# Kernel optimization log

Hardware: AMD Instinct MI355X
Metric: run time of the kernel (lower is better)

Reference implementation:

```python
import jax, jax.numpy as jnp
import numpy as np

N_NODES = 20000
N_EDGES = 320000
N_GRAPHS = 64
SEQ = 20
SCALAR = 16
EMB = 32
HID = 128
HEADS = 4
IN_DIM = SCALAR + 5 * EMB  # 176
NEG_SLOPE = 0.2


def masked_mean_embed(table, idx):
    # table: [V, EMB], idx: [N, L] with 0 = padding
    emb = table[idx]                                  # [N, L, EMB]
    mask = (idx != 0).astype(emb.dtype)[..., None]    # [N, L, 1]
    return (emb * mask).sum(axis=1) / (mask.sum(axis=1) + 1e-9)


def gat_conv(x, src, dst, W, att_src, att_dst, bias, heads, out_ch):
    # PyG GATConv (add_self_loops already applied to src/dst), concat heads.
    N = x.shape[0]
    xw = (x @ W).reshape(N, heads, out_ch)            # [N, H, C]
    a_src = (xw * att_src).sum(-1)                    # [N, H]
    a_dst = (xw * att_dst).sum(-1)                    # [N, H]
    e = jax.nn.leaky_relu(a_src[src] + a_dst[dst], NEG_SLOPE)  # [E, H]
    e_max = jax.ops.segment_max(e, dst, num_segments=N)
    e_max = jnp.where(jnp.isfinite(e_max), e_max, 0.0)
    ex = jnp.exp(e - e_max[dst])                      # [E, H]
    denom = jax.ops.segment_sum(ex, dst, num_segments=N)
    alpha = ex / (denom[dst] + 1e-16)                 # [E, H]
    msg = xw[src] * alpha[:, :, None]                 # [E, H, C]
    out = jax.ops.segment_sum(msg, dst, num_segments=N)
    return out.reshape(N, heads * out_ch) + bias


def setup_inputs() -> dict:
    key = jax.random.key(0)
    ks = jax.random.split(key, 24)
    s = 0.05
    inp = {
        "x_scalar": jax.random.normal(ks[0], (N_NODES, SCALAR), jnp.float32),
        "x_opcode": jax.random.randint(ks[1], (N_NODES, SEQ), 0, 256),
        "x_source": jax.random.randint(ks[2], (N_NODES, SEQ), 0, 512),
        "x_sink": jax.random.randint(ks[3], (N_NODES, SEQ), 0, 512),
        "x_string_manip": jax.random.randint(ks[4], (N_NODES, SEQ), 0, 128),
        "x_payload": jax.random.randint(ks[5], (N_NODES, SEQ), 0, 1024),
        "edge_index": jax.random.randint(ks[6], (2, N_EDGES), 0, N_NODES),
        "batch": jnp.sort(jax.random.randint(ks[7], (N_NODES,), 0, N_GRAPHS)),
        # embedding tables (row 0 = padding; masked out anyway)
        "emb_opcode": jax.random.normal(ks[8], (256, EMB)) * s,
        "emb_source": jax.random.normal(ks[9], (512, EMB)) * s,
        "emb_sink": jax.random.normal(ks[10], (512, EMB)) * s,
        "emb_string": jax.random.normal(ks[11], (128, EMB)) * s,
        "emb_payload": jax.random.normal(ks[12], (1024, EMB)) * s,
        "ln_gamma": jnp.ones((IN_DIM,), jnp.float32),
        "ln_beta": jnp.zeros((IN_DIM,), jnp.float32),
        "W1": jax.random.normal(ks[13], (IN_DIM, HEADS * HID)) * s,
        "att_src1": jax.random.normal(ks[14], (HEADS, HID)) * s,
        "att_dst1": jax.random.normal(ks[15], (HEADS, HID)) * s,
        "b1": jnp.zeros((HEADS * HID,), jnp.float32),
        "W2": jax.random.normal(ks[16], (HEADS * HID, HID)) * s,
        "att_src2": jax.random.normal(ks[17], (1, HID)) * s,
        "att_dst2": jax.random.normal(ks[18], (1, HID)) * s,
        "b2": jnp.zeros((HID,), jnp.float32),
        "cls_w1": jax.random.normal(ks[19], (HID, HID // 2)) * s,
        "cls_b1": jnp.zeros((HID // 2,), jnp.float32),
        "cls_w2": jax.random.normal(ks[20], (HID // 2, 2)) * s,
        "cls_b2": jnp.zeros((2,), jnp.float32),
    }
    return inp


def reference(x_scalar, x_opcode, x_source, x_sink, x_string_manip, x_payload,
              edge_index, batch,
              emb_opcode, emb_source, emb_sink, emb_string, emb_payload,
              ln_gamma, ln_beta,
              W1, att_src1, att_dst1, b1,
              W2, att_src2, att_dst2, b2,
              cls_w1, cls_b1, cls_w2, cls_b2):
    feats = jnp.concatenate([
        x_scalar,
        masked_mean_embed(emb_opcode, x_opcode),
        masked_mean_embed(emb_source, x_source),
        masked_mean_embed(emb_sink, x_sink),
        masked_mean_embed(emb_string, x_string_manip),
        masked_mean_embed(emb_payload, x_payload),
    ], axis=1)  # [N, 176]
    mu = feats.mean(-1, keepdims=True)
    var = ((feats - mu) ** 2).mean(-1, keepdims=True)
    h = (feats - mu) / jnp.sqrt(var + 1e-5) * ln_gamma + ln_beta

    # add self loops (PyG GATConv default)
    loops = jnp.arange(N_NODES, dtype=edge_index.dtype)
    src = jnp.concatenate([edge_index[0], loops])
    dst = jnp.concatenate([edge_index[1], loops])

    x = jax.nn.elu(gat_conv(h, src, dst, W1, att_src1, att_dst1, b1, HEADS, HID))
    x = jax.nn.elu(gat_conv(x, src, dst, W2, att_src2, att_dst2, b2, 1, HID))

    pooled = jax.ops.segment_max(x, batch, num_segments=N_GRAPHS)  # [G, HID]
    hcls = jax.nn.relu(pooled @ cls_w1 + cls_b1)
    return hcls @ cls_w2 + cls_b2  # [G, 2]
```

## Files before the change

### kernel.cpp

```cpp
#include <hip/hip_runtime.h>
#include <hip/hip_bf16.h>
#include <math.h>

#define N_NODES 20000
#define N_EDGES 320000
#define N_GRAPHS 64
#define SEQ 20
#define SCALAR 16
#define EMB 32
#define HID 128
#define IN_DIM 176
#define TOT_EDGES (N_EDGES + N_NODES)
#define CHUNK_SMALL 10000
#define POOL_SLICES 32

typedef _Float16 half8v __attribute__((ext_vector_type(8)));
typedef float f32x4 __attribute__((ext_vector_type(4)));
#define LO_SCALE 2048.0f
#define LO_INV (1.0f / 2048.0f)

#define PB2_ELEMS (16 * 8 * 64 * 8)
#define PB1_ELEMS (4 * 6 * 8 * 64 * 8)

#define COUNT_BLOCKS ((TOT_EDGES + 255) / 256)
#define NB4 ((N_NODES + 3) / 4)
#define L1_PACK1 NB4
#define L1_PACK2 (NB4 + 48)
#define L1_COUNT (NB4 + 80)
#define L1_TOTAL (NB4 + 80 + COUNT_BLOCKS + 1)

__device__ inline float readlane_f(float v, int l) {
  return __uint_as_float(__builtin_amdgcn_readlane(__float_as_uint(v), l));
}
__device__ inline int readlane_i(int v, int l) {
  return __builtin_amdgcn_readlane(v, l);
}
__device__ inline float leaky(float e) { return e >= 0.f ? e : 0.2f * e; }
__device__ inline float elu(float v) { return v > 0.f ? v : expf(v) - 1.f; }

__global__ __launch_bounds__(256) void wasd_kernel(
    const float* __restrict__ W1, const float* __restrict__ att_s1,
    const float* __restrict__ att_d1, float* __restrict__ was4,
    float* __restrict__ wad4) {
  int lane = threadIdx.x & 63;
  int k = blockIdx.x * 4 + (threadIdx.x >> 6);
  if (k >= IN_DIM) return;
  const float* wrow = W1 + (size_t)k * 512;
  float s[4], d[4];
#pragma unroll
  for (int hh = 0; hh < 4; ++hh) {
    float w0 = wrow[hh * 128 + lane], w1 = wrow[hh * 128 + 64 + lane];
    float a0 = att_s1[hh * 128 + lane], a1 = att_s1[hh * 128 + 64 + lane];
    float c0 = att_d1[hh * 128 + lane], c1 = att_d1[hh * 128 + 64 + lane];
    s[hh] = w0 * a0 + w1 * a1;
    d[hh] = w0 * c0 + w1 * c1;
  }
  for (int off = 1; off < 64; off <<= 1) {
#pragma unroll
    for (int hh = 0; hh < 4; ++hh) {
      s[hh] += __shfl_xor(s[hh], off);
      d[hh] += __shfl_xor(d[hh], off);
    }
  }
  if (lane == 0) {
    *(float4*)&was4[k * 4] = make_float4(s[0], s[1], s[2], s[3]);
    *(float4*)&wad4[k * 4] = make_float4(d[0], d[1], d[2], d[3]);
  }
}

__global__ __launch_bounds__(256) void feats_setup_kernel(
    const float* __restrict__ xs,
    const int* __restrict__ i0, const int* __restrict__ i1,
    const int* __restrict__ i2, const int* __restrict__ i3,
    const int* __restrict__ i4,
    const float* __restrict__ t0, const float* __restrict__ t1,
    const float* __restrict__ t2, const float* __restrict__ t3,
    const float* __restrict__ t4,
    const float* __restrict__ gamma, const float* __restrict__ beta,
    const float* __restrict__ was4, const float* __restrict__ wad4,
    const float* __restrict__ W1, const float* __restrict__ W2,
    const int* __restrict__ edge_index, const int* __restrict__ batch,
    float* __restrict__ hout, float* __restrict__ a_s,
    float* __restrict__ a_d,
    _Float16* __restrict__ PB1h, _Float16* __restrict__ PB1l,
    _Float16* __restrict__ PB2h, _Float16* __restrict__ PB2l,
    int* __restrict__ cnt, int* __restrict__ gstarts) {
  int b = blockIdx.x;
  if (b >= NB4) {
    if (b < L1_PACK2) {
      int t = (b - L1_PACK1) * 256 + threadIdx.x;
      int lane = t & 63, wi = t >> 6;
      int r = lane & 15, g = lane >> 4;
      int ntile = wi & 7, rem = wi >> 3;
      int ks = rem % 6, hh = rem / 6;
      int col = hh * 128 + ntile * 16 + r;
      size_t o = ((size_t)wi * 64 + lane) * 8;
#pragma unroll
      for (int j = 0; j < 8; ++j) {
        int k = ks * 32 + g * 8 + j;
        float v = (k < IN_DIM) ? W1[(size_t)k * 512 + col] : 0.f;
        _Float16 h = (_Float16)v;
        PB1h[o + j] = h;
        PB1l[o + j] = (_Float16)((v - (float)h) * LO_SCALE);
      }
    } else if (b < L1_COUNT) {
      int t = (b - L1_PACK2) * 256 + threadIdx.x;
      int lane = t & 63, wi = t >> 6;
      int r = lane & 15, g = lane >> 4;
      int ks = wi >> 3, ntile = wi & 7;
      int col = ntile * 16 + r;
      size_t o = ((size_t)wi * 64 + lane) * 8;
#pragma unroll
      for (int j = 0; j < 8; ++j) {
        int k = ks * 32 + g * 8 + j;
        float v = W2[(size_t)k * 128 + col];
        _Float16 h = (_Float16)v;
        PB2h[o + j] = h;
        PB2l[o + j] = (_Float16)((v - (float)h) * LO_SCALE);
      }
    } else if (b < L1_COUNT + COUNT_BLOCKS) {
      int i = (b - L1_COUNT) * 256 + threadIdx.x;
      if (i < N_EDGES) {
        atomicAdd(&cnt[edge_index[N_EDGES + i]], 1);
      } else if (i < TOT_EDGES) {
        atomicAdd(&cnt[i - N_EDGES], 1);
      }
    } else {
      int t = threadIdx.x;
      if (t > N_GRAPHS) return;
      int lo = 0, hi = N_NODES;
      while (lo < hi) {
        int mid = (lo + hi) >> 1;
        if (batch[mid] < t) lo = mid + 1; else hi = mid;
      }
      gstarts[t] = lo;
    }
    return;
  }
  int lane = threadIdx.x & 63;
  int w = threadIdx.x >> 6;
  int n = b * 4 + w;
  if (n >= N_NODES) return;
  __shared__ int sidx[4][100];
  {
    int j = lane;
    int tab = j / 20, l = j - tab * 20;
    const int* ip = tab == 0 ? i0 : tab == 1 ? i1 : tab == 2 ? i2 : i3;
    sidx[w][j] = ip[n * SEQ + l];
    if (lane < 36) {
      int j2 = 64 + lane;
      int tab2 = j2 / 20, l2 = j2 - tab2 * 20;
      const int* ip2 = tab2 == 3 ? i3 : i4;
      sidx[w][j2] = ip2[n * SEQ + l2];
    }
  }
  bool l48 = lane < 48;
  float f0, f1, f2 = 0.f;
  if (lane < SCALAR) {
    f0 = xs[n * SCALAR + lane];
  } else {
    int tt = lane - SCALAR, tab = tt >> 5, d = tt & 31;
    const float* tp = tab == 0 ? t0 : t1;
    float sum = 0.f, cnt2 = 0.f;
#pragma unroll
    for (int l = 0; l < SEQ; ++l) {
      int id = sidx[w][tab * 20 + l];
      if (id != 0) { sum += tp[id * EMB + d]; cnt2 += 1.f; }
    }
    f0 = sum / (cnt2 + 1e-9f);
  }
  {
    int tt = 48 + lane, tab = tt >> 5, d = tt & 31;
    const float* tp = tab == 1 ? t1 : tab == 2 ? t2 : t3;
    float sum = 0.f, cnt2 = 0.f;
#pragma unroll
    for (int l = 0; l < SEQ; ++l) {
      int id = sidx[w][tab * 20 + l];
      if (id != 0) { sum += tp[id * EMB + d]; cnt2 += 1.f; }
    }
    f1 = sum / (cnt2 + 1e-9f);
  }
  if (l48) {
    int tt = 112 + lane, tab = tt >> 5, d = tt & 31;
    const float* tp = tab == 3 ? t3 : t4;
    float sum = 0.f, cnt2 = 0.f;
#pragma unroll
    for (int l = 0; l < SEQ; ++l) {
      int id = sidx[w][tab * 20 + l];
      if (id != 0) { sum += tp[id * EMB + d]; cnt2 += 1.f; }
    }
    f2 = sum / (cnt2 + 1e-9f);
  }
  float s = f0 + f1 + f2;
  for (int off = 1; off < 64; off <<= 1) s += __shfl_xor(s, off);
  float mu = s / (float)IN_DIM;
  float v = (f0 - mu) * (f0 - mu) + (f1 - mu) * (f1 - mu) +
            (l48 ? (f2 - mu) * (f2 - mu) : 0.f);
  for (int off = 1; off < 64; off <<= 1) v += __shfl_xor(v, off);
  float rstd = 1.0f / sqrtf(v / (float)IN_DIM + 1e-5f);
  float hv0 = (f0 - mu) * rstd * gamma[lane] + beta[lane];
  float hv1 = (f1 - mu) * rstd * gamma[64 + lane] + beta[64 + lane];
  float hv2 = l48 ? (f2 - mu) * rstd * gamma[128 + lane] + beta[128 + lane] : 0.f;
  float* hr = hout + (size_t)n * IN_DIM;
  hr[lane] = hv0;
  hr[64 + lane] = hv1;
  if (l48) hr[128 + lane] = hv2;

  const float4* wsv = (const float4*)was4;
  const float4* wdv = (const float4*)wad4;
  float4 wsa = wsv[lane], wsb = wsv[64 + lane];
  float4 wsc = l48 ? wsv[128 + lane] : make_float4(0.f, 0.f, 0.f, 0.f);
  float4 wda = wdv[lane], wdb = wdv[64 + lane];
  float4 wdc = l48 ? wdv[128 + lane] : make_float4(0.f, 0.f, 0.f, 0.f);
  float ps0 = hv0 * wsa.x + hv1 * wsb.x + hv2 * wsc.x;
  float ps1 = hv0 * wsa.y + hv1 * wsb.y + hv2 * wsc.y;
  float ps2 = hv0 * wsa.z + hv1 * wsb.z + hv2 * wsc.z;
  float ps3 = hv0 * wsa.w + hv1 * wsb.w + hv2 * wsc.w;
  float pd0 = hv0 * wda.x + hv1 * wdb.x + hv2 * wdc.x;
  float pd1 = hv0 * wda.y + hv1 * wdb.y + hv2 * wdc.y;
  float pd2 = hv0 * wda.z + hv1 * wdb.z + hv2 * wdc.z;
  float pd3 = hv0 * wda.w + hv1 * wdb.w + hv2 * wdc.w;
  for (int off = 1; off < 64; off <<= 1) {
    ps0 += __shfl_xor(ps0, off); ps1 += __shfl_xor(ps1, off);
    ps2 += __shfl_xor(ps2, off); ps3 += __shfl_xor(ps3, off);
    pd0 += __shfl_xor(pd0, off); pd1 += __shfl_xor(pd1, off);
    pd2 += __shfl_xor(pd2, off); pd3 += __shfl_xor(pd3, off);
  }
  if (lane == 0) {
    *(float4*)&a_s[n * 4] = make_float4(ps0, ps1, ps2, ps3);
    *(float4*)&a_d[n * 4] = make_float4(pd0, pd1, pd2, pd3);
  }
}

__global__ __launch_bounds__(1024) void prefix_kernel(const int* __restrict__ cnt,
                                                      int* __restrict__ indptr,
                                                      int n, int total) {
  __shared__ int ss[1024];
  int t = threadIdx.x;
  int per = (n + 1023) / 1024;
  int beg = t * per, end = min(beg + per, n);
  int s = 0;
  for (int i = beg; i < end; ++i) s += cnt[i];
  ss[t] = s;
  __syncthreads();
  for (int off = 1; off < 1024; off <<= 1) {
    int v = (t >= off) ? ss[t - off] : 0;
    __syncthreads();
    ss[t] += v;
    __syncthreads();
  }
  int run = ss[t] - s;
  for (int i = beg; i < end; ++i) { indptr[i] = run; run += cnt[i]; }
  if (t == 0) indptr[n] = total;
}

__global__ void scatter_kernel(const int* __restrict__ edge_index,
                               const int* __restrict__ indptr,
                               int* __restrict__ cursor,
                               int* __restrict__ srcs) {
  int i = blockIdx.x * 256 + threadIdx.x;
  int s, d;
  if (i < N_EDGES) { s = edge_index[i]; d = edge_index[N_EDGES + i]; }
  else if (i < TOT_EDGES) { s = i - N_EDGES; d = s; }
  else return;
  int pos = indptr[d] + atomicAdd(&cursor[d], 1);
  srcs[pos] = s;
}

__global__ __launch_bounds__(256) void agg1h_kernel(
    const float* __restrict__ h, const float* __restrict__ a_src,
    const float* __restrict__ a_dst, const int* __restrict__ indptr,
    const int* __restrict__ srcs, _Float16* __restrict__ agghh,
    _Float16* __restrict__ agghl, int n0, int nM) {
  int lane = threadIdx.x & 63;
  int ln = blockIdx.x * 4 + (threadIdx.x >> 6);
  if (ln >= nM) return;
  int n = n0 + ln;
  int beg = indptr[n], end = indptr[n + 1];
  int deg = end - beg;
  float4 ad = *(const float4*)&a_dst[n * 4];
  bool l48 = lane < 48;
  float acc[4][3] = {};

  auto body = [&](int s, float al0, float al1, float al2, float al3) {
    const float* r = h + (size_t)s * IN_DIM;
    float v0 = r[lane];
    float v1 = r[64 + lane];
    float v2 = l48 ? r[128 + lane] : 0.f;
    acc[0][0] += al0 * v0; acc[0][1] += al0 * v1; acc[0][2] += al0 * v2;
    acc[1][0] += al1 * v0; acc[1][1] += al1 * v1; acc[1][2] += al1 * v2;
    acc[2][0] += al2 * v0; acc[2][1] += al2 * v1; acc[2][2] += al2 * v2;
    acc[3][0] += al3 * v0; acc[3][1] += al3 * v1; acc[3][2] += al3 * v2;
  };
  auto walk4 = [&](int s, float al0, float al1, float al2, float al3, int jn) {
    int jj = 0;
    for (; jj + 4 <= jn; jj += 4) {
      int sa = readlane_i(s, jj), sb = readlane_i(s, jj + 1);
      int sc = readlane_i(s, jj + 2), sd = readlane_i(s, jj + 3);
      float a0 = readlane_f(al0, jj), a1 = readlane_f(al1, jj);
      float a2 = readlane_f(al2, jj), a3 = readlane_f(al3, jj);
      float b0 = readlane_f(al0, jj + 1), b1 = readlane_f(al1, jj + 1);
      float b2 = readlane_f(al2, jj + 1), b3 = readlane_f(al3, jj + 1);
      float c0 = readlane_f(al0, jj + 2), c1 = readlane_f(al1, jj + 2);
      float c2 = readlane_f(al2, jj + 2), c3 = readlane_f(al3, jj + 2);
      float d0 = readlane_f(al0, jj + 3), d1 = readlane_f(al1, jj + 3);
      float d2 = readlane_f(al2, jj + 3), d3 = readlane_f(al3, jj + 3);
      body(sa, a0, a1, a2, a3);
      body(sb, b0, b1, b2, b3);
      body(sc, c0, c1, c2, c3);
      body(sd, d0, d1, d2, d3);
    }
    for (; jj < jn; ++jj) {
      int sa = readlane_i(s, jj);
      body(sa, readlane_f(al0, jj), readlane_f(al1, jj),
           readlane_f(al2, jj), readlane_f(al3, jj));
    }
  };

  if (deg <= 64) {
    int j = beg + lane;
    int s = 0;
    float e0 = -INFINITY, e1 = -INFINITY, e2 = -INFINITY, e3 = -INFINITY;
    if (j < end) {
      s = srcs[j];
      float4 as = *(const float4*)&a_src[s * 4];
      e0 = leaky(as.x + ad.x); e1 = leaky(as.y + ad.y);
      e2 = leaky(as.z + ad.z); e3 = leaky(as.w + ad.w);
    }
    float m0 = e0, m1 = e1, m2 = e2, m3 = e3;
    for (int off = 1; off < 64; off <<= 1) {
      m0 = fmaxf(m0, __shfl_xor(m0, off)); m1 = fmaxf(m1, __shfl_xor(m1, off));
      m2 = fmaxf(m2, __shfl_xor(m2, off)); m3 = fmaxf(m3, __shfl_xor(m3, off));
    }
    float x0 = (j < end) ? expf(e0 - m0) : 0.f;
    float x1 = (j < end) ? expf(e1 - m1) : 0.f;
    float x2 = (j < end) ? expf(e2 - m2) : 0.f;
    float x3 = (j < end) ? expf(e3 - m3) : 0.f;
    float d0 = x0, d1 = x1, d2 = x2, d3 = x3;
    for (int off = 1; off < 64; off <<= 1) {
      d0 += __shfl_xor(d0, off); d1 += __shfl_xor(d1, off);
      d2 += __shfl_xor(d2, off); d3 += __shfl_xor(d3, off);
    }
    float al0 = x0 / (d0 + 1e-16f), al1 = x1 / (d1 + 1e-16f);
    float al2 = x2 / (d2 + 1e-16f), al3 = x3 / (d3 + 1e-16f);
    walk4(s, al0, al1, al2, al3, deg);
  } else {
    float m0 = -INFINITY, m1 = -INFINITY, m2 = -INFINITY, m3 = -INFINITY;
    for (int j0 = beg; j0 < end; j0 += 64) {
      int j = j0 + lane;
      if (j < end) {
        int s = srcs[j];
        float4 as = *(const float4*)&a_src[s * 4];
        m0 = fmaxf(m0, leaky(as.x + ad.x)); m1 = fmaxf(m1, leaky(as.y + ad.y));
        m2 = fmaxf(m2, leaky(as.z + ad.z)); m3 = fmaxf(m3, leaky(as.w + ad.w));
      }
    }
    for (int off = 1; off < 64; off <<= 1) {
      m0 = fmaxf(m0, __shfl_xor(m0, off)); m1 = fmaxf(m1, __shfl_xor(m1, off));
      m2 = fmaxf(m2, __shfl_xor(m2, off)); m3 = fmaxf(m3, __shfl_xor(m3, off));
    }
    float d0 = 0.f, d1 = 0.f, d2 = 0.f, d3 = 0.f;
    for (int j0 = beg; j0 < end; j0 += 64) {
      int j = j0 + lane;
      if (j < end) {
        int s = srcs[j];
        float4 as = *(const float4*)&a_src[s * 4];
        d0 += expf(leaky(as.x + ad.x) - m0); d1 += expf(leaky(as.y + ad.y) - m1);
        d2 += expf(leaky(as.z + ad.z) - m2); d3 += expf(leaky(as.w + ad.w) - m3);
      }
    }
    for (int off = 1; off < 64; off <<= 1) {
      d0 += __shfl_xor(d0, off); d1 += __shfl_xor(d1, off);
      d2 += __shfl_xor(d2, off); d3 += __shfl_xor(d3, off);
    }
    float r0 = 1.f / (d0 + 1e-16f), r1 = 1.f / (d1 + 1e-16f);
    float r2 = 1.f / (d2 + 1e-16f), r3 = 1.f / (d3 + 1e-16f);
    for (int j0 = beg; j0 < end; j0 += 64) {
      int jn = min(64, end - j0);
      int j = j0 + lane;
      int s = 0;
      float al0 = 0.f, al1 = 0.f, al2 = 0.f, al3 = 0.f;
      if (j < end) {
        s = srcs[j];
        float4 as = *(const float4*)&a_src[s * 4];
        al0 = expf(leaky(as.x + ad.x) - m0) * r0;
        al1 = expf(leaky(as.y + ad.y) - m1) * r1;
        al2 = expf(leaky(as.z + ad.z) - m2) * r2;
        al3 = expf(leaky(as.w + ad.w) - m3) * r3;
      }
      walk4(s, al0, al1, al2, al3, jn);
    }
  }

  size_t base = (size_t)ln * (4 * IN_DIM);
#pragma unroll
  for (int hh = 0; hh < 4; ++hh) {
    size_t o0 = base + hh * IN_DIM + lane;
    float v0 = acc[hh][0], v1 = acc[hh][1];
    _Float16 h0 = (_Float16)v0, h1 = (_Float16)v1;
    agghh[o0] = h0;      agghl[o0] = (_Float16)((v0 - (float)h0) * LO_SCALE);
    agghh[o0 + 64] = h1; agghl[o0 + 64] = (_Float16)((v1 - (float)h1) * LO_SCALE);
    if (l48) {
      float v2 = acc[hh][2];
      _Float16 h2 = (_Float16)v2;
      agghh[o0 + 128] = h2;
      agghl[o0 + 128] = (_Float16)((v2 - (float)h2) * LO_SCALE);
    }
  }
}

__global__ __launch_bounds__(512) void gemm_fused_kernel(
    const _Float16* __restrict__ Ah, const _Float16* __restrict__ Al,
    const half8v* __restrict__ PB1h, const half8v* __restrict__ PB1l,
    const float* __restrict__ b1,
    const half8v* __restrict__ PB2h, const half8v* __restrict__ PB2l,
    const float* __restrict__ att_s, const float* __restrict__ att_d,
    float* __restrict__ xw2, float* __restrict__ a_s, float* __restrict__ a_d,
    int n0, int nM) {
  __shared__ _Float16 s1h[32][520];
  __shared__ _Float16 s1l[32][520];
  int lane = threadIdx.x & 63;
  int w = threadIdx.x >> 6;
  int rows0 = blockIdx.x * 32;
  if (rows0 >= nM) return;
  int r = lane & 15, g = lane >> 4;
  int r1 = (rows0 + 16 + r < nM) ? (rows0 + 16 + r) : (rows0 + r);

  {
    int hh = w >> 1, colhalf = w & 1;
    f32x4 acc[2][4] = {};
    f32x4 accm[2][4] = {};
    const _Float16* a0h = Ah + ((size_t)(rows0 + r) * 4 + hh) * IN_DIM;
    const _Float16* a0l = Al + ((size_t)(rows0 + r) * 4 + hh) * IN_DIM;
    const _Float16* a1h = Ah + ((size_t)r1 * 4 + hh) * IN_DIM;
    const _Float16* a1l = Al + ((size_t)r1 * 4 + hh) * IN_DIM;
#pragma unroll 2
    for (int ks = 0; ks < 6; ++ks) {
      int kg = ks * 32 + g * 8;
      int koff = (kg + 8 <= IN_DIM) ? kg : 0;
      half8v ah0 = *(const half8v*)(a0h + koff);
      half8v al0 = *(const half8v*)(a0l + koff);
      half8v ah1 = *(const half8v*)(a1h + koff);
      half8v al1 = *(const half8v*)(a1l + koff);
      const half8v* bh = PB1h + (size_t)(((hh * 6 + ks) * 8 + colhalf * 4) * 64) + lane;
      const half8v* bl = PB1l + (size_t)(((hh * 6 + ks) * 8 + colhalf * 4) * 64) + lane;
#pragma unroll
      for (int nt = 0; nt < 4; ++nt) {
        half8v bhv = bh[nt * 64], blv = bl[nt * 64];
        accm[0][nt] = __builtin_amdgcn_mfma_f32_16x16x32_f16(al0, bhv, accm[0][nt], 0, 0, 0);
        accm[0][nt] = __builtin_amdgcn_mfma_f32_16x16x32_f16(ah0, blv, accm[0][nt], 0, 0, 0);
        acc[0][nt]  = __builtin_amdgcn_mfma_f32_16x16x32_f16(ah0, bhv, acc[0][nt], 0, 0, 0);
        accm[1][nt] = __builtin_amdgcn_mfma_f32_16x16x32_f16(al1, bhv, accm[1][nt], 0, 0, 0);
        accm[1][nt] = __builtin_amdgcn_mfma_f32_16x16x32_f16(ah1, blv, accm[1][nt], 0, 0, 0);
        acc[1][nt]  = __builtin_amdgcn_mfma_f32_16x16x32_f16(ah1, bhv, acc[1][nt], 0, 0, 0);
      }
    }
#pragma unroll
    for (int nt = 0; nt < 4; ++nt) {
      int col = hh * 128 + colhalf * 64 + nt * 16 + r;
      float bb = b1[col];
#pragma unroll
      for (int mt = 0; mt < 2; ++mt) {
#pragma unroll
        for (int i = 0; i < 4; ++i) {
          int row = mt * 16 + g * 4 + i;
          if (rows0 + row < nM) {
            float o = elu(acc[mt][nt][i] + accm[mt][nt][i] * LO_INV + bb);
            _Float16 oh = (_Float16)o;
            s1h[row][col] = oh;
            s1l[row][col] = (_Float16)((o - (float)oh) * LO_SCALE);
          }
        }
      }
    }
  }
  __syncthreads();

  {
    f32x4 qacc[2] = {};
    f32x4 qaccm[2] = {};
#pragma unroll 2
    for (int ks = 0; ks < 16; ++ks) {
      half8v ah0 = *(const half8v*)&s1h[r][ks * 32 + g * 8];
      half8v al0 = *(const half8v*)&s1l[r][ks * 32 + g * 8];
      half8v ah1 = *(const half8v*)&s1h[16 + r][ks * 32 + g * 8];
      half8v al1 = *(const half8v*)&s1l[16 + r][ks * 32 + g * 8];
      half8v bhv = PB2h[(size_t)((ks * 8 + w) * 64) + lane];
      half8v blv = PB2l[(size_t)((ks * 8 + w) * 64) + lane];
      qaccm[0] = __builtin_amdgcn_mfma_f32_16x16x32_f16(al0, bhv, qaccm[0], 0, 0, 0);
      qaccm[0] = __builtin_amdgcn_mfma_f32_16x16x32_f16(ah0, blv, qaccm[0], 0, 0, 0);
      qacc[0]  = __builtin_amdgcn_mfma_f32_16x16x32_f16(ah0, bhv, qacc[0], 0, 0, 0);
      qaccm[1] = __builtin_amdgcn_mfma_f32_16x16x32_f16(al1, bhv, qaccm[1], 0, 0, 0);
      qaccm[1] = __builtin_amdgcn_mfma_f32_16x16x32_f16(ah1, blv, qaccm[1], 0, 0, 0);
      qacc[1]  = __builtin_amdgcn_mfma_f32_16x16x32_f16(ah1, bhv, qacc[1], 0, 0, 0);
    }
    int col = w * 16 + r;
    float as_ = att_s[col], ad_ = att_d[col];
    float ps[2][4], pd[2][4];
#pragma unroll
    for (int mt = 0; mt < 2; ++mt) {
#pragma unroll
      for (int i = 0; i < 4; ++i) {
        float v = qacc[mt][i] + qaccm[mt][i] * LO_INV;
        int row = rows0 + mt * 16 + g * 4 + i;
        if (row < nM) xw2[(size_t)(n0 + row) * 128 + col] = v;
        ps[mt][i] = v * as_;
        pd[mt][i] = v * ad_;
      }
    }
#pragma unroll
    for (int mt = 0; mt < 2; ++mt) {
#pragma unroll
      for (int i = 0; i < 4; ++i) {
        for (int off = 1; off < 16; off <<= 1) {
          ps[mt][i] += __shfl_xor(ps[mt][i], off);
          pd[mt][i] += __shfl_xor(pd[mt][i], off);
        }
      }
    }
    if (r == 0) {
#pragma unroll
      for (int mt = 0; mt < 2; ++mt) {
#pragma unroll
        for (int i = 0; i < 4; ++i) {
          int row = rows0 + mt * 16 + g * 4 + i;
          if (row < nM) {
            atomicAdd(&a_s[n0 + row], ps[mt][i]);
            atomicAdd(&a_d[n0 + row], pd[mt][i]);
          }
        }
      }
    }
  }
}

__global__ __launch_bounds__(256) void agg2_kernel(
    const float* __restrict__ xw, const float* __restrict__ a_src,
    const float* __restrict__ a_dst, const int* __restrict__ indptr,
    const int* __restrict__ srcs, const float* __restrict__ bias,
    float* __restrict__ out) {
  int lane = threadIdx.x & 63;
  int n = blockIdx.x * 4 + (threadIdx.x >> 6);
  if (n >= N_NODES) return;
  int beg = indptr[n], end = indptr[n + 1];
  int deg = end - beg;
  float adn = a_dst[n];
  int half = lane >> 5, l32 = lane & 31;
  float4 acc = make_float4(0.f, 0.f, 0.f, 0.f);

  auto quads = [&](int s, float al, int jn) {
    int jj = 0;
    for (; jj + 4 <= jn; jj += 4) {
      int s0 = readlane_i(s, jj), s1 = readlane_i(s, jj + 1);
      int s2 = readlane_i(s, jj + 2), s3 = readlane_i(s, jj + 3);
      float a0 = readlane_f(al, jj), a1 = readlane_f(al, jj + 1);
      float a2 = readlane_f(al, jj + 2), a3 = readlane_f(al, jj + 3);
      int sh0 = half ? s1 : s0;   float ah0 = half ? a1 : a0;
      int sh1 = half ? s3 : s2;   float ah1 = half ? a3 : a2;
      float4 v0 = *(const float4*)&xw[(size_t)sh0 * HID + l32 * 4];
      float4 v1 = *(const float4*)&xw[(size_t)sh1 * HID + l32 * 4];
      acc.x += ah0 * v0.x; acc.y += ah0 * v0.y;
      acc.z += ah0 * v0.z; acc.w += ah0 * v0.w;
      acc.x += ah1 * v1.x; acc.y += ah1 * v1.y;
      acc.z += ah1 * v1.z; acc.w += ah1 * v1.w;
    }
    for (; jj + 2 <= jn; jj += 2) {
      int sa = readlane_i(s, jj), sb = readlane_i(s, jj + 1);
      float aa = readlane_f(al, jj), ab = readlane_f(al, jj + 1);
      int sh = half ? sb : sa;
      float ahx = half ? ab : aa;
      float4 v = *(const float4*)&xw[(size_t)sh * HID + l32 * 4];
      acc.x += ahx * v.x; acc.y += ahx * v.y; acc.z += ahx * v.z; acc.w += ahx * v.w;
    }
    if (jj < jn) {
      int sa = readlane_i(s, jj);
      float ahx = half ? 0.f : readlane_f(al, jj);
      float4 v = *(const float4*)&xw[(size_t)sa * HID + l32 * 4];
      acc.x += ahx * v.x; acc.y += ahx * v.y; acc.z += ahx * v.z; acc.w += ahx * v.w;
    }
  };

  if (deg <= 64) {
    int j = beg + lane;
    int s = 0;
    float e = -INFINITY;
    if (j < end) { s = srcs[j]; e = leaky(a_src[s] + adn); }
    float m = e;
    for (int off = 1; off < 64; off <<= 1) m = fmaxf(m, __shfl_xor(m, off));
    float x = (j < end) ? expf(e - m) : 0.f;
    float d = x;
    for (int off = 1; off < 64; off <<= 1) d += __shfl_xor(d, off);
    float al = x / (d + 1e-16f);
    quads(s, al, deg);
  } else {
    float m = -INFINITY;
    for (int j0 = beg; j0 < end; j0 += 64) {
      int j = j0 + lane;
      if (j < end) m = fmaxf(m, leaky(a_src[srcs[j]] + adn));
    }
    for (int off = 1; off < 64; off <<= 1) m = fmaxf(m, __shfl_xor(m, off));
    float d = 0.f;
    for (int j0 = beg; j0 < end; j0 += 64) {
      int j = j0 + lane;
      if (j < end) d += expf(leaky(a_src[srcs[j]] + adn) - m);
    }
    for (int off = 1; off < 64; off <<= 1) d += __shfl_xor(d, off);
    float rd = 1.f / (d + 1e-16f);
    for (int j0 = beg; j0 < end; j0 += 64) {
      int jn = min(64, end - j0);
      int j = j0 + lane;
      int s = 0;
      float al = 0.f;
      if (j < end) {
        s = srcs[j];
        al = expf(leaky(a_src[s] + adn) - m) * rd;
      }
      quads(s, al, jn);
    }
  }

  acc.x += __shfl_xor(acc.x, 32); acc.y += __shfl_xor(acc.y, 32);
  acc.z += __shfl_xor(acc.z, 32); acc.w += __shfl_xor(acc.w, 32);
  if (half == 0) {
    float4 b = *(const float4*)&bias[l32 * 4];
    float4 o;
    o.x = elu(acc.x + b.x); o.y = elu(acc.y + b.y);
    o.z = elu(acc.z + b.z); o.w = elu(acc.w + b.w);
    *(float4*)&out[(size_t)n * HID + l32 * 4] = o;
  }
}

__global__ __launch_bounds__(HID) void pool_part_kernel(
    const float* __restrict__ out2, const int* __restrict__ gstarts,
    float* __restrict__ part) {
  int g = blockIdx.x, s = blockIdx.y, t = threadIdx.x;
  int beg = gstarts[g], end = gstarts[g + 1];
  int len = end - beg;
  int b0 = beg + (int)(((long long)len * s) / POOL_SLICES);
  int b1 = beg + (int)(((long long)len * (s + 1)) / POOL_SLICES);
  float m = -INFINITY;
  for (int n = b0; n < b1; ++n) m = fmaxf(m, out2[(size_t)n * HID + t]);
  part[((size_t)g * POOL_SLICES + s) * HID + t] = m;
}

__global__ __launch_bounds__(HID) void pool_reduce_kernel(
    const float* __restrict__ part, float* __restrict__ pooled) {
  int g = blockIdx.x, t = threadIdx.x;
  float m = -INFINITY;
#pragma unroll
  for (int s = 0; s < POOL_SLICES; ++s)
    m = fmaxf(m, part[((size_t)g * POOL_SLICES + s) * HID + t]);
  pooled[g * HID + t] = m;
}

__global__ __launch_bounds__(HID) void cls_kernel(const float* __restrict__ pooled,
                                                  const float* __restrict__ w1,
                                                  const float* __restrict__ b1,
                                                  const float* __restrict__ w2,
                                                  const float* __restrict__ b2,
                                                  float* __restrict__ out) {
  int g = blockIdx.x, t = threadIdx.x;
  __shared__ float sp[HID], sh1[HID / 2];
  sp[t] = pooled[g * HID + t];
  __syncthreads();
  if (t < HID / 2) {
    float s = b1[t];
    for (int k = 0; k < HID; ++k) s += sp[k] * w1[k * (HID / 2) + t];
    sh1[t] = fmaxf(s, 0.f);
  }
  __syncthreads();
  if (t < 2) {
    float o = b2[t];
    for (int k = 0; k < HID / 2; ++k) o += sh1[k] * w2[k * 2 + t];
    out[g * 2 + t] = o;
  }
}

extern "C" void kernel_launch(void* const* d_in, const int* in_sizes, int n_in,
                              void* d_out, int out_size, void* d_ws, size_t ws_size,
                              hipStream_t stream) {
  const float* x_scalar = (const float*)d_in[0];
  const int* x_opcode   = (const int*)d_in[1];
  const int* x_source   = (const int*)d_in[2];
  const int* x_sink     = (const int*)d_in[3];
  const int* x_string   = (const int*)d_in[4];
  const int* x_payload  = (const int*)d_in[5];
  const int* edge_index = (const int*)d_in[6];
  const int* batch      = (const int*)d_in[7];
  const float* emb_opcode = (const float*)d_in[8];
  const float* emb_source = (const float*)d_in[9];
  const float* emb_sink   = (const float*)d_in[10];
  const float* emb_string = (const float*)d_in[11];
  const float* emb_payload= (const float*)d_in[12];
  const float* ln_gamma = (const float*)d_in[13];
  const float* ln_beta  = (const float*)d_in[14];
  const float* W1       = (const float*)d_in[15];
  const float* att_src1 = (const float*)d_in[16];
  const float* att_dst1 = (const float*)d_in[17];
  const float* b1       = (const float*)d_in[18];
  const float* W2       = (const float*)d_in[19];
  const float* att_src2 = (const float*)d_in[20];
  const float* att_dst2 = (const float*)d_in[21];
  const float* b2       = (const float*)d_in[22];
  const float* cls_w1   = (const float*)d_in[23];
  const float* cls_b1   = (const float*)d_in[24];
  const float* cls_w2   = (const float*)d_in[25];
  const float* cls_b2   = (const float*)d_in[26];

  auto total_bytes = [&](int chunk) -> size_t {
    size_t f = (size_t)N_NODES * IN_DIM + (size_t)N_NODES * HID * 2 +
               N_NODES * 4 * 2 + N_NODES * 2 + IN_DIM * 4 * 2 + N_GRAPHS * HID;
    size_t ii = (N_NODES + 1) + N_NODES * 2 + TOT_EDGES + (N_GRAPHS + 1);
    size_t f16b = ((size_t)2 * (PB2_ELEMS + PB1_ELEMS) +
                   (size_t)chunk * 4 * IN_DIM * 2) * sizeof(_Float16) + 64;
    size_t poolb = (size_t)N_GRAPHS * POOL_SLICES * HID * 4 + 32;
    return f * 4 + ii * 4 + f16b + poolb + 256;
  };
  int chunk = (ws_size >= total_bytes(N_NODES)) ? N_NODES : CHUNK_SMALL;

  float* h      = (float*)d_ws;
  _Float16* agghh = (_Float16*)(h + (size_t)N_NODES * IN_DIM);
  _Float16* agghl = agghh + (size_t)chunk * 4 * IN_DIM;
  float* xw2    = (float*)(agghl + (size_t)chunk * 4 * IN_DIM);
  float* out2   = xw2 + (size_t)N_NODES * HID;
  float* a1s    = out2 + (size_t)N_NODES * HID;
  float* a1d    = a1s + N_NODES * 4;
  float* was4   = a1d + N_NODES * 4;
  float* wad4   = was4 + IN_DIM * 4;
  float* pooled = wad4 + IN_DIM * 4;
  int* indptr = (int*)(pooled + N_GRAPHS * HID);
  int* cnt    = indptr + (N_NODES + 1);
  int* cursor = cnt + N_NODES;
  float* a2s  = (float*)(cursor + N_NODES);
  float* a2d  = a2s + N_NODES;
  int* srcs   = (int*)(a2d + N_NODES);
  int* gstarts= srcs + TOT_EDGES;
  uintptr_t pal = ((uintptr_t)(gstarts + N_GRAPHS + 1) + 15) & ~(uintptr_t)15;
  _Float16* PB2h = (_Float16*)pal;
  _Float16* PB2l = PB2h + PB2_ELEMS;
  _Float16* PB1h = PB2l + PB2_ELEMS;
  _Float16* PB1l = PB1h + PB1_ELEMS;
  uintptr_t ppal = ((uintptr_t)(PB1l + PB1_ELEMS) + 15) & ~(uintptr_t)15;
  float* pool_part = (float*)ppal;

  hipMemsetAsync(cnt, 0, 4 * N_NODES * sizeof(int), stream);

  wasd_kernel<<<(IN_DIM + 3) / 4, 256, 0, stream>>>(W1, att_src1, att_dst1,
                                                    was4, wad4);

  feats_setup_kernel<<<L1_TOTAL, 256, 0, stream>>>(
      x_scalar, x_opcode, x_source, x_sink, x_string, x_payload,
      emb_opcode, emb_source, emb_sink, emb_string, emb_payload,
      ln_gamma, ln_beta, was4, wad4, W1, W2, edge_index, batch,
      h, a1s, a1d, PB1h, PB1l, PB2h, PB2l, cnt, gstarts);

  prefix_kernel<<<1, 1024, 0, stream>>>(cnt, indptr, N_NODES, TOT_EDGES);

  scatter_kernel<<<COUNT_BLOCKS, 256, 0, stream>>>(edge_index, indptr, cursor,
                                                   srcs);

  for (int n0 = 0; n0 < N_NODES; n0 += chunk) {
    int nM = min(chunk, N_NODES - n0);
    agg1h_kernel<<<(nM + 3) / 4, 256, 0, stream>>>(h, a1s, a1d, indptr, srcs,
                                                   agghh, agghl, n0, nM);
    gemm_fused_kernel<<<(nM + 31) / 32, 512, 0, stream>>>(
        agghh, agghl, (const half8v*)PB1h, (const half8v*)PB1l, b1,
        (const half8v*)PB2h, (const half8v*)PB2l, att_src2, att_dst2,
        xw2, a2s, a2d, n0, nM);
  }

  agg2_kernel<<<NB4, 256, 0, stream>>>(xw2, a2s, a2d, indptr, srcs, b2, out2);

  pool_part_kernel<<<dim3(N_GRAPHS, POOL_SLICES), HID, 0, stream>>>(out2, gstarts, pool_part);
  pool_reduce_kernel<<<N_GRAPHS, HID, 0, stream>>>(pool_part, pooled);
  cls_kernel<<<N_GRAPHS, HID, 0, stream>>>(pooled, cls_w1, cls_b1, cls_w2, cls_b2, (float*)d_out);
}
```

Before: 350.5 us.

## Fuse graph max-pooling into agg2 via order-preserving atomicMax encoding

Replaces the out2 buffer and the two-stage pool_part/pool_reduce kernels with atomicMax on an order-preserving unsigned encoding of floats, performed directly in the agg2 epilogue. The pooled buffer is zeroed by extending the existing memset; zero decodes below any real value. This removes a 10 MB write and re-read plus two kernel launches and the gstarts binary search. In exchange it adds contended atomics, since about 312 nodes per graph hit the same 128 addresses.

```diff
diff --git a/kernel.cpp b/kernel.cpp
--- a/kernel.cpp
+++ b/kernel.cpp
@@ -12,7 +12,6 @@
 #define IN_DIM 176
 #define TOT_EDGES (N_EDGES + N_NODES)
 #define CHUNK_SMALL 10000
-#define POOL_SLICES 32
 
 typedef _Float16 half8v __attribute__((ext_vector_type(8)));
 typedef float f32x4 __attribute__((ext_vector_type(4)));
@@ -27,7 +26,7 @@
 #define L1_PACK1 NB4
 #define L1_PACK2 (NB4 + 48)
 #define L1_COUNT (NB4 + 80)
-#define L1_TOTAL (NB4 + 80 + COUNT_BLOCKS + 1)
+#define L1_TOTAL (NB4 + 80 + COUNT_BLOCKS)
 
 __device__ inline float readlane_f(float v, int l) {
   return __uint_as_float(__builtin_amdgcn_readlane(__float_as_uint(v), l));
@@ -37,6 +36,14 @@
 }
 __device__ inline float leaky(float e) { return e >= 0.f ? e : 0.2f * e; }
 __device__ inline float elu(float v) { return v > 0.f ? v : expf(v) - 1.f; }
+
+__device__ inline unsigned encf(float x) {
+  unsigned b = __float_as_uint(x);
+  return (b & 0x80000000u) ? ~b : (b | 0x80000000u);
+}
+__device__ inline float decf(unsigned e) {
+  return __uint_as_float((e & 0x80000000u) ? (e & 0x7FFFFFFFu) : ~e);
+}
 
 __global__ __launch_bounds__(256) void wasd_kernel(
     const float* __restrict__ W1, const float* __restrict__ att_s1,
@@ -79,12 +86,12 @@
     const float* __restrict__ gamma, const float* __restrict__ beta,
     const float* __restrict__ was4, const float* __restrict__ wad4,
     const float* __restrict__ W1, const float* __restrict__ W2,
-    const int* __restrict__ edge_index, const int* __restrict__ batch,
+    const int* __restrict__ edge_index,
     float* __restrict__ hout, float* __restrict__ a_s,
     float* __restrict__ a_d,
     _Float16* __restrict__ PB1h, _Float16* __restrict__ PB1l,
     _Float16* __restrict__ PB2h, _Float16* __restrict__ PB2l,
-    int* __restrict__ cnt, int* __restrict__ gstarts) {
+    int* __restrict__ cnt) {
   int b = blockIdx.x;
   if (b >= NB4) {
     if (b < L1_PACK2) {
@@ -118,22 +125,13 @@
         PB2h[o + j] = h;
         PB2l[o + j] = (_Float16)((v - (float)h) * LO_SCALE);
       }
-    } else if (b < L1_COUNT + COUNT_BLOCKS) {
+    } else {
       int i = (b - L1_COUNT) * 256 + threadIdx.x;
       if (i < N_EDGES) {
         atomicAdd(&cnt[edge_index[N_EDGES + i]], 1);
       } else if (i < TOT_EDGES) {
         atomicAdd(&cnt[i - N_EDGES], 1);
       }
-    } else {
-      int t = threadIdx.x;
-      if (t > N_GRAPHS) return;
-      int lo = 0, hi = N_NODES;
-      while (lo < hi) {
-        int mid = (lo + hi) >> 1;
-        if (batch[mid] < t) lo = mid + 1; else hi = mid;
-      }
-      gstarts[t] = lo;
     }
     return;
   }
@@ -538,7 +536,7 @@
     const float* __restrict__ xw, const float* __restrict__ a_src,
     const float* __restrict__ a_dst, const int* __restrict__ indptr,
     const int* __restrict__ srcs, const float* __restrict__ bias,
-    float* __restrict__ out) {
+    const int* __restrict__ batch, unsigned* __restrict__ pooled_u) {
   int lane = threadIdx.x & 63;
   int n = blockIdx.x * 4 + (threadIdx.x >> 6);
   if (n >= N_NODES) return;
@@ -623,37 +621,16 @@
   acc.z += __shfl_xor(acc.z, 32); acc.w += __shfl_xor(acc.w, 32);
   if (half == 0) {
     float4 b = *(const float4*)&bias[l32 * 4];
-    float4 o;
-    o.x = elu(acc.x + b.x); o.y = elu(acc.y + b.y);
-    o.z = elu(acc.z + b.z); o.w = elu(acc.w + b.w);
-    *(float4*)&out[(size_t)n * HID + l32 * 4] = o;
-  }
-}
-
-__global__ __launch_bounds__(HID) void pool_part_kernel(
-    const float* __restrict__ out2, const int* __restrict__ gstarts,
-    float* __restrict__ part) {
-  int g = blockIdx.x, s = blockIdx.y, t = threadIdx.x;
-  int beg = gstarts[g], end = gstarts[g + 1];
-  int len = end - beg;
-  int b0 = beg + (int)(((long long)len * s) / POOL_SLICES);
-  int b1 = beg + (int)(((long long)len * (s + 1)) / POOL_SLICES);
-  float m = -INFINITY;
-  for (int n = b0; n < b1; ++n) m = fmaxf(m, out2[(size_t)n * HID + t]);
-  part[((size_t)g * POOL_SLICES + s) * HID + t] = m;
-}
-
-__global__ __launch_bounds__(HID) void pool_reduce_kernel(
-    const float* __restrict__ part, float* __restrict__ pooled) {
-  int g = blockIdx.x, t = threadIdx.x;
-  float m = -INFINITY;
-#pragma unroll
-  for (int s = 0; s < POOL_SLICES; ++s)
-    m = fmaxf(m, part[((size_t)g * POOL_SLICES + s) * HID + t]);
-  pooled[g * HID + t] = m;
-}
-
-__global__ __launch_bounds__(HID) void cls_kernel(const float* __restrict__ pooled,
+    int g = batch[n];
+    unsigned* p = &pooled_u[(size_t)g * HID + l32 * 4];
+    atomicMax(&p[0], encf(elu(acc.x + b.x)));
+    atomicMax(&p[1], encf(elu(acc.y + b.y)));
+    atomicMax(&p[2], encf(elu(acc.z + b.z)));
+    atomicMax(&p[3], encf(elu(acc.w + b.w)));
+  }
+}
+
+__global__ __launch_bounds__(HID) void cls_kernel(const unsigned* __restrict__ pooled_u,
                                                   const float* __restrict__ w1,
                                                   const float* __restrict__ b1,
                                                   const float* __restrict__ w2,
@@ -661,7 +638,7 @@
                                                   float* __restrict__ out) {
   int g = blockIdx.x, t = threadIdx.x;
   __shared__ float sp[HID], sh1[HID / 2];
-  sp[t] = pooled[g * HID + t];
+  sp[t] = decf(pooled_u[(size_t)g * HID + t]);
   __syncthreads();
   if (t < HID / 2) {
     float s = b1[t];
@@ -708,13 +685,12 @@
   const float* cls_b2   = (const float*)d_in[26];
 
   auto total_bytes = [&](int chunk) -> size_t {
-    size_t f = (size_t)N_NODES * IN_DIM + (size_t)N_NODES * HID * 2 +
-               N_NODES * 4 * 2 + N_NODES * 2 + IN_DIM * 4 * 2 + N_GRAPHS * HID;
-    size_t ii = (N_NODES + 1) + N_NODES * 2 + TOT_EDGES + (N_GRAPHS + 1);
+    size_t f = (size_t)N_NODES * IN_DIM + (size_t)N_NODES * HID +
+               N_NODES * 4 * 2 + N_NODES * 2 + IN_DIM * 4 * 2;
+    size_t ii = (N_NODES + 1) + N_NODES * 2 + TOT_EDGES + N_GRAPHS * HID;
     size_t f16b = ((size_t)2 * (PB2_ELEMS + PB1_ELEMS) +
                    (size_t)chunk * 4 * IN_DIM * 2) * sizeof(_Float16) + 64;
-    size_t poolb = (size_t)N_GRAPHS * POOL_SLICES * HID * 4 + 32;
-    return f * 4 + ii * 4 + f16b + poolb + 256;
+    return f * 4 + ii * 4 + f16b + 256;
   };
   int chunk = (ws_size >= total_bytes(N_NODES)) ? N_NODES : CHUNK_SMALL;
 
@@ -722,28 +698,25 @@
   _Float16* agghh = (_Float16*)(h + (size_t)N_NODES * IN_DIM);
   _Float16* agghl = agghh + (size_t)chunk * 4 * IN_DIM;
   float* xw2    = (float*)(agghl + (size_t)chunk * 4 * IN_DIM);
-  float* out2   = xw2 + (size_t)N_NODES * HID;
-  float* a1s    = out2 + (size_t)N_NODES * HID;
+  float* a1s    = xw2 + (size_t)N_NODES * HID;
   float* a1d    = a1s + N_NODES * 4;
   float* was4   = a1d + N_NODES * 4;
   float* wad4   = was4 + IN_DIM * 4;
-  float* pooled = wad4 + IN_DIM * 4;
-  int* indptr = (int*)(pooled + N_GRAPHS * HID);
+  int* indptr = (int*)(wad4 + IN_DIM * 4);
   int* cnt    = indptr + (N_NODES + 1);
   int* cursor = cnt + N_NODES;
   float* a2s  = (float*)(cursor + N_NODES);
   float* a2d  = a2s + N_NODES;
-  int* srcs   = (int*)(a2d + N_NODES);
-  int* gstarts= srcs + TOT_EDGES;
-  uintptr_t pal = ((uintptr_t)(gstarts + N_GRAPHS + 1) + 15) & ~(uintptr_t)15;
+  unsigned* pooled_u = (unsigned*)(a2d + N_NODES);
+  int* srcs   = (int*)(pooled_u + N_GRAPHS * HID);
+  uintptr_t pal = ((uintptr_t)(srcs + TOT_EDGES) + 15) & ~(uintptr_t)15;
   _Float16* PB2h = (_Float16*)pal;
   _Float16* PB2l = PB2h + PB2_ELEMS;
   _Float16* PB1h = PB2l + PB2_ELEMS;
   _Float16* PB1l = PB1h + PB1_ELEMS;
-  uintptr_t ppal = ((uintptr_t)(PB1l + PB1_ELEMS) + 15) & ~(uintptr_t)15;
-  float* pool_part = (float*)ppal;
-
-  hipMemsetAsync(cnt, 0, 4 * N_NODES * sizeof(int), stream);
+
+  hipMemsetAsync(cnt, 0, (4 * (size_t)N_NODES + N_GRAPHS * HID) * sizeof(int),
+                 stream);
 
   wasd_kernel<<<(IN_DIM + 3) / 4, 256, 0, stream>>>(W1, att_src1, att_dst1,
                                                     was4, wad4);
@@ -751,8 +724,8 @@
   feats_setup_kernel<<<L1_TOTAL, 256, 0, stream>>>(
       x_scalar, x_opcode, x_source, x_sink, x_string, x_payload,
       emb_opcode, emb_source, emb_sink, emb_string, emb_payload,
-      ln_gamma, ln_beta, was4, wad4, W1, W2, edge_index, batch,
-      h, a1s, a1d, PB1h, PB1l, PB2h, PB2l, cnt, gstarts);
+      ln_gamma, ln_beta, was4, wad4, W1, W2, edge_index,
+      h, a1s, a1d, PB1h, PB1l, PB2h, PB2l, cnt);
 
   prefix_kernel<<<1, 1024, 0, stream>>>(cnt, indptr, N_NODES, TOT_EDGES);
 
@@ -769,9 +742,9 @@
         xw2, a2s, a2d, n0, nM);
   }
 
-  agg2_kernel<<<NB4, 256, 0, stream>>>(xw2, a2s, a2d, indptr, srcs, b2, out2);
-
-  pool_part_kernel<<<dim3(N_GRAPHS, POOL_SLICES), HID, 0, stream>>>(out2, gstarts, pool_part);
-  pool_reduce_kernel<<<N_GRAPHS, HID, 0, stream>>>(pool_part, pooled);
-  cls_kernel<<<N_GRAPHS, HID, 0, stream>>>(pooled, cls_w1, cls_b1, cls_w2, cls_b2, (float*)d_out);
-}
+  agg2_kernel<<<NB4, 256, 0, stream>>>(xw2, a2s, a2d, indptr, srcs, b2,
+                                       batch, pooled_u);
+
+  cls_kernel<<<N_GRAPHS, HID, 0, stream>>>(pooled_u, cls_w1, cls_b1, cls_w2,
+                                           cls_b2, (float*)d_out);
+}
```

Measured after the change: 410.1 us. 1.17x slower.
